# Kernel tuning notes

Hardware: AMD Instinct MI355X
Metric: run time of the kernel (lower is better)

## Reference

```python
import jax, jax.numpy as jnp
import numpy as np

NODE_TYPES = ["patient", "visit", "symptom", "procedure", "disease", "drug"]
N = {"patient": 20000, "visit": 100000, "symptom": 4000, "procedure": 8000,
     "disease": 10000, "drug": 4000}
D = 128          # embedding_dim == hidden_channels
N_LAYERS = 4     # conv1..conv4
# (src, dst) per relation; reverse edges included so every node type gets messages
REL = [("patient", "visit"), ("visit", "patient"),
       ("visit", "symptom"), ("symptom", "visit"),
       ("visit", "procedure"), ("procedure", "visit"),
       ("visit", "disease"), ("disease", "visit"),
       ("visit", "drug"), ("drug", "visit")]
E_FWD = {("patient", "visit"): 100000, ("visit", "symptom"): 300000,
         ("visit", "procedure"): 200000, ("visit", "disease"): 250000,
         ("visit", "drug"): 300000}
EI_NAMES = ["ei_pv", "ei_vp", "ei_vs", "ei_sv", "ei_vpr", "ei_prv",
            "ei_vd", "ei_dv", "ei_vdr", "ei_drv"]
E_LABEL = 200000


def setup_inputs() -> dict:
    key = jax.random.key(0)
    ks = iter(jax.random.split(key, 64))
    inp = {}
    for nt in NODE_TYPES:
        inp[f"node_id_{nt}"] = jnp.arange(N[nt], dtype=jnp.int32)
        inp[f"emb_{nt}"] = jax.random.normal(next(ks), (N[nt], D), jnp.float32)
    for name, (src, dst) in zip(EI_NAMES, REL):
        e = E_FWD.get((src, dst), E_FWD.get((dst, src)))
        row = jax.random.randint(next(ks), (e,), 0, N[src], dtype=jnp.int32)
        col = jax.random.randint(next(ks), (e,), 0, N[dst], dtype=jnp.int32)
        inp[name] = jnp.stack([row, col])
    R = len(REL)
    inp["W_l"] = jax.random.normal(next(ks), (N_LAYERS, R, D, D), jnp.float32) * 0.05
    inp["b_l"] = jnp.zeros((N_LAYERS, R, D), jnp.float32)
    inp["W_r"] = jax.random.normal(next(ks), (N_LAYERS, R, D, D), jnp.float32) * 0.05
    inp["cls_w1"] = jax.random.normal(next(ks), (2 * D, D), jnp.float32) * 0.05
    inp["cls_b1"] = jnp.zeros((D,), jnp.float32)
    inp["cls_w2"] = jax.random.normal(next(ks), (D, 1), jnp.float32) * 0.05
    inp["cls_b2"] = jnp.zeros((1,), jnp.float32)
    row = jax.random.randint(next(ks), (E_LABEL,), 0, N["visit"], dtype=jnp.int32)
    col = jax.random.randint(next(ks), (E_LABEL,), 0, N["drug"], dtype=jnp.int32)
    inp["edge_label_index"] = jnp.stack([row, col])
    inp["edge_label"] = jax.random.bernoulli(next(ks), 0.5, (E_LABEL,)).astype(jnp.float32)
    return inp


def _hetero_sage_layer(x, eis, Wl, bl, Wr):
    # to_hetero semantics: out[dst] = sum over edge types (src,rel,dst) of
    #   SAGEConv_rel: lin_l(mean_j x[src][j]) + lin_r(x[dst])   (PyG defaults)
    out = {nt: jnp.zeros_like(v) for nt, v in x.items()}
    for r, (src, dst) in enumerate(REL):
        ei = eis[r]
        n_dst = x[dst].shape[0]
        msg = jax.ops.segment_sum(x[src][ei[0]], ei[1], num_segments=n_dst)
        deg = jax.ops.segment_sum(jnp.ones((ei.shape[1],), x[src].dtype), ei[1],
                                  num_segments=n_dst)
        mean = msg / jnp.maximum(deg, 1.0)[:, None]  # empty segments stay 0 as in PyG
        out[dst] = out[dst] + mean @ Wl[r] + bl[r] + x[dst] @ Wr[r]
    return out


def reference(node_id_patient, node_id_visit, node_id_symptom, node_id_procedure,
              node_id_disease, node_id_drug,
              emb_patient, emb_visit, emb_symptom, emb_procedure, emb_disease, emb_drug,
              ei_pv, ei_vp, ei_vs, ei_sv, ei_vpr, ei_prv, ei_vd, ei_dv, ei_vdr, ei_drv,
              W_l, b_l, W_r, cls_w1, cls_b1, cls_w2, cls_b2,
              edge_label_index, edge_label):
    x = {"patient": emb_patient[node_id_patient],
         "visit": emb_visit[node_id_visit],
         "symptom": emb_symptom[node_id_symptom],
         "procedure": emb_procedure[node_id_procedure],
         "disease": emb_disease[node_id_disease],
         "drug": emb_drug[node_id_drug]}
    eis = [ei_pv, ei_vp, ei_vs, ei_sv, ei_vpr, ei_prv, ei_vd, ei_dv, ei_vdr, ei_drv]
    for l in range(N_LAYERS):
        x = _hetero_sage_layer(x, eis, W_l[l], b_l[l], W_r[l])
        if l < N_LAYERS - 1:  # relu after conv1..conv3 only; dropout is eval-mode identity
            x = {k: jax.nn.relu(v) for k, v in x.items()}
    # Classifier: gather visit/drug node features per labeled edge, concat, MLP
    zv = x["visit"][edge_label_index[0]]
    zd = x["drug"][edge_label_index[1]]
    h = jax.nn.relu(jnp.concatenate([zv, zd], axis=-1) @ cls_w1 + cls_b1)
    pred = (h @ cls_w2 + cls_b2).reshape(-1)
    # BCE with logits: softplus(z) - z*y, mean-reduced
    loss = jnp.mean(jax.nn.softplus(pred) - pred * edge_label)
    return loss, pred
```

## Files before the change

kernel.cpp:

```cpp
#include <hip/hip_runtime.h>
#include <cmath>


typedef _Float16 f16x8 __attribute__((ext_vector_type(8)));
typedef _Float16 f16x4 __attribute__((ext_vector_type(4)));
typedef float f32x4 __attribute__((ext_vector_type(4)));

#define NREL 10
#define NCOUNTS 546000
#define NEDGES  2300000
#define NVISIT  100000
#define NVEDGES 1150000
#define PLW 546816
#define WT_ELEMS (4 * PLW + 67584)
#define XELEMS 18688000UL
#define SELEMS 5888000UL
#define NBKT 873
#define BCAP 5120

struct GatherMeta { const float* emb[6]; const int* nid[6]; int rows[6]; int off[6]; };
struct AggMeta { const int* rp[5]; _Float16* meanH[5]; _Float16* meanL[5]; int M[5]; };
struct BkMeta {
  const int* ei[NREL]; int E[NREL]; int cbc[NREL]; int ndst[NREL];
  int sh[NREL]; int bb[NREL]; int nb[NREL];
};
struct MTask {
  const _Float16* AH0; const _Float16* AL0;
  const _Float16* AH1; const _Float16* AL1;
  const _Float16* W;
  const float* bias;
  _Float16* outH; _Float16* outL;
  int M, blkOff, K, relu;
};
struct MMeta { MTask t[6]; int nTasks; };

__global__ __launch_bounds__(256) void conv0(GatherMeta g, _Float16* __restrict__ H,
                                             _Float16* __restrict__ L) {
  int t = blockIdx.y;
  int i = blockIdx.x * 256 + threadIdx.x;
  if (i >= g.rows[t] * 16) return;
  int row = i >> 4, q = i & 15;
  int s = g.nid[t][row];
  const float* p = g.emb[t] + (size_t)s * 128 + q * 8;
  float4 v0 = *(const float4*)p;
  float4 v1 = *(const float4*)(p + 4);
  float v[8] = {v0.x, v0.y, v0.z, v0.w, v1.x, v1.y, v1.z, v1.w};
  f16x8 h, l;
  #pragma unroll
  for (int j = 0; j < 8; ++j) {
    h[j] = (_Float16)v[j];
    l[j] = (_Float16)(v[j] - (float)h[j]);
  }
  size_t o = (size_t)(g.off[t] + row) * 128 + q * 8;
  *(f16x8*)(H + o) = h;
  *(f16x8*)(L + o) = l;
}

__global__ __launch_bounds__(256) void bkt_p1(BkMeta bm, int* __restrict__ bcur,
                                              int* __restrict__ bdata) {
  __shared__ int cnt[128];
  __shared__ int base[128];
  __shared__ unsigned short rnk[4096];
  int r = blockIdx.y;
  int E = bm.E[r], sh = bm.sh[r], bb = bm.bb[r], nb = bm.nb[r];
  int tid = threadIdx.x;
  if (tid < 128) cnt[tid] = 0;
  __syncthreads();
  int e0 = blockIdx.x * 4096;
  if (e0 >= E) return;
  const int* dstp = bm.ei[r] + E;
  const int* srcp = bm.ei[r];
  #pragma unroll
  for (int i = 0; i < 16; ++i) {
    int e = e0 + i * 256 + tid;
    if (e < E) {
      int b = dstp[e] >> sh;
      rnk[i * 256 + tid] = (unsigned short)atomicAdd(&cnt[b], 1);
    }
  }
  __syncthreads();
  if (tid < nb && cnt[tid] > 0) base[tid] = atomicAdd(&bcur[bb + tid], cnt[tid]);
  __syncthreads();
  #pragma unroll
  for (int i = 0; i < 16; ++i) {
    int e = e0 + i * 256 + tid;
    if (e < E) {
      int d = dstp[e];
      int b = d >> sh;
      int pos = base[b] + (int)rnk[i * 256 + tid];
      if (pos < BCAP)
        bdata[(size_t)(bb + b) * BCAP + pos] = ((d & ((1 << sh) - 1)) << 17) | srcp[e];
    }
  }
}

__global__ __launch_bounds__(256) void bkt_p2a(BkMeta bm, const int* __restrict__ bcur,
                                               const int* __restrict__ bdata,
                                               int* __restrict__ counts) {
  __shared__ int hist[2048];
  int g = blockIdx.x;
  int r = 0;
  #pragma unroll
  for (int i = 1; i < NREL; ++i) if (g >= bm.bb[i]) r = i;
  int lb = g - bm.bb[r];
  int sh = bm.sh[r], dpb = 1 << sh;
  int tid = threadIdx.x;
  for (int d = tid; d < dpb; d += 256) hist[d] = 0;
  __syncthreads();
  int cnt = bcur[g]; if (cnt > BCAP) cnt = BCAP;
  const int* bd = bdata + (size_t)g * BCAP;
  for (int i = tid; i < cnt; i += 256) atomicAdd(&hist[((unsigned)bd[i]) >> 17], 1);
  __syncthreads();
  int dBase = lb << sh;
  int dMax = bm.ndst[r] - dBase; if (dMax > dpb) dMax = dpb;
  for (int d = tid; d < dMax; d += 256) counts[bm.cbc[r] + dBase + d] = hist[d];
}

__global__ __launch_bounds__(1024) void scan1(const int* __restrict__ counts,
                                              int* __restrict__ partials) {
  __shared__ int s[1024];
  int i = blockIdx.x * 1024 + threadIdx.x;
  s[threadIdx.x] = (i < NCOUNTS) ? counts[i] : 0;
  __syncthreads();
  for (int off = 512; off > 0; off >>= 1) {
    if (threadIdx.x < off) s[threadIdx.x] += s[threadIdx.x + off];
    __syncthreads();
  }
  if (threadIdx.x == 0) partials[blockIdx.x] = s[0];
}

__global__ __launch_bounds__(1024) void scan2(int* __restrict__ partials, int nb) {
  __shared__ int s[1024];
  int t = threadIdx.x;
  int v = (t < nb) ? partials[t] : 0;
  s[t] = v;
  __syncthreads();
  for (int off = 1; off < 1024; off <<= 1) {
    int add = (t >= off) ? s[t - off] : 0;
    __syncthreads();
    s[t] += add;
    __syncthreads();
  }
  if (t < nb) partials[t] = s[t] - v;
}

__global__ __launch_bounds__(1024) void scan3(const int* __restrict__ counts,
                                              int* __restrict__ prefix,
                                              const int* __restrict__ partials) {
  __shared__ int s[1024];
  int t = threadIdx.x;
  int i = blockIdx.x * 1024 + t;
  int v = (i < NCOUNTS) ? counts[i] : 0;
  s[t] = v;
  __syncthreads();
  for (int off = 1; off < 1024; off <<= 1) {
    int add = (t >= off) ? s[t - off] : 0;
    __syncthreads();
    s[t] += add;
    __syncthreads();
  }
  int P = partials[blockIdx.x] + s[t] - v;
  if (i < NCOUNTS) prefix[i] = P;
  if (blockIdx.x == 0 && t == 0) prefix[NCOUNTS] = NEDGES;
}

__global__ __launch_bounds__(256) void bkt_p2b(BkMeta bm, const int* __restrict__ bcur,
                                               const int* __restrict__ bdata,
                                               const int* __restrict__ prefix,
                                               int* __restrict__ esrc) {
  __shared__ int pk[BCAP];
  __shared__ int srt[BCAP];
  __shared__ int cur[2048];
  __shared__ int part[256];
  __shared__ int baseSh;
  int g = blockIdx.x;
  int r = 0;
  #pragma unroll
  for (int i = 1; i < NREL; ++i) if (g >= bm.bb[i]) r = i;
  int lb = g - bm.bb[r];
  int sh = bm.sh[r], dpb = 1 << sh;
  int tid = threadIdx.x;
  int cnt = bcur[g]; if (cnt > BCAP) cnt = BCAP;
  const int* bd = bdata + (size_t)g * BCAP;
  for (int d = tid; d < dpb; d += 256) cur[d] = 0;
  for (int i = tid; i < cnt; i += 256) pk[i] = bd[i];
  __syncthreads();
  for (int i = tid; i < cnt; i += 256) atomicAdd(&cur[((unsigned)pk[i]) >> 17], 1);
  __syncthreads();
  int seg = (dpb + 255) >> 8;
  int s = 0;
  int b0 = tid * seg;
  for (int j = 0; j < seg; ++j) {
    int idx = b0 + j;
    if (idx < dpb) { int v = cur[idx]; cur[idx] = s; s += v; }
  }
  part[tid] = s;
  __syncthreads();
  for (int off = 1; off < 256; off <<= 1) {
    int add = (tid >= off) ? part[tid - off] : 0;
    __syncthreads();
    part[tid] += add;
    __syncthreads();
  }
  int myoff = part[tid] - s;
  for (int j = 0; j < seg; ++j) {
    int idx = b0 + j;
    if (idx < dpb) cur[idx] += myoff;
  }
  if (tid == 0) baseSh = prefix[bm.cbc[r] + (lb << sh)];
  __syncthreads();
  for (int i = tid; i < cnt; i += 256) {
    int p = pk[i];
    int pos = atomicAdd(&cur[((unsigned)p) >> 17], 1);
    srt[pos] = p & 0x1FFFF;
  }
  __syncthreads();
  int base = baseSh;
  for (int i = tid; i < cnt; i += 256) esrc[base + i] = srt[i];
}

__global__ __launch_bounds__(256) void merge_visit(const int* __restrict__ prefix,
                                                   const int* __restrict__ esrc,
                                                   int* __restrict__ mprefix,
                                                   int2* __restrict__ mesrc) {
  const int cbc[5]  = {0, 124000, 232000, 342000, 446000};
  const int yoff[5] = {0, 20000, 24000, 32000, 42000};
  int v = blockIdx.x * 256 + threadIdx.x;
  if (v >= NVISIT) return;
  int e0[5], e1[5];
  int base = 0;
  #pragma unroll
  for (int q = 0; q < 5; ++q) {
    e0[q] = prefix[cbc[q] + v];
    e1[q] = prefix[cbc[q] + v + 1];
    base += e0[q] - prefix[cbc[q]];
  }
  mprefix[v] = base;
  if (v == NVISIT - 1) {
    int t = base;
    #pragma unroll
    for (int q = 0; q < 5; ++q) t += e1[q] - e0[q];
    mprefix[NVISIT] = t;
  }
  int pos = base;
  #pragma unroll
  for (int q = 0; q < 5; ++q) {
    int d = e1[q] - e0[q];
    if (d > 0) {
      int wb = __float_as_int(1.f / (float)d);
      for (int e = e0[q]; e < e1[q]; ++e)
        mesrc[pos++] = make_int2(yoff[q] + esrc[e], wb);
    }
  }
}

__global__ __launch_bounds__(256) void prep_split(
    const float* __restrict__ W_l, const float* __restrict__ b_l,
    const float* __restrict__ W_r, const float* __restrict__ cw1,
    _Float16* __restrict__ Wt, float* __restrict__ visitSumB) {
  const int visitRel[5] = {0, 3, 5, 7, 9};
  const int inRel[5] = {1, 2, 4, 6, 8};
  int gid = blockIdx.x * 256 + threadIdx.x;
  if (gid < 1048576) {
    int l = gid >> 18, o = gid & 262143;
    float val; size_t base; int n, k, Kpad;
    if (o < 163840) {
      int t = o >> 15, e = o & 32767;
      k = e >> 7; n = e & 127; Kpad = 264;
      int r = inRel[t];
      val = (k < 128) ? W_l[(size_t)(l * 10 + r) * 16384 + k * 128 + n]
                      : W_r[(size_t)(l * 10 + r) * 16384 + (k - 128) * 128 + n];
      base = (size_t)l * PLW + t * 67584;
    } else if (o < 245760) {
      int q = (o - 163840) >> 14, e = (o - 163840) & 16383;
      k = e >> 7; n = e & 127; Kpad = 136;
      val = W_l[(size_t)(l * 10 + visitRel[q]) * 16384 + k * 128 + n];
      base = (size_t)l * PLW + 337920 + q * 34816;
    } else {
      int e = o - 245760;
      k = e >> 7; n = e & 127; Kpad = 136;
      val = 0.f;
      #pragma unroll
      for (int q = 0; q < 5; ++q)
        val += W_r[(size_t)(l * 10 + visitRel[q]) * 16384 + k * 128 + n];
      base = (size_t)l * PLW + 512000;
    }
    _Float16 h = (_Float16)val;
    _Float16 lo = (_Float16)(val - (float)h);
    Wt[base + (size_t)n * Kpad + k] = h;
    Wt[base + (size_t)(128 + n) * Kpad + k] = lo;
  } else if (gid < 1081344) {
    int e = gid - 1048576;
    int k = e >> 7, n = e & 127;
    float val = cw1[(size_t)k * 128 + n];
    _Float16 h = (_Float16)val;
    _Float16 lo = (_Float16)(val - (float)h);
    size_t base = (size_t)4 * PLW;
    Wt[base + (size_t)n * 264 + k] = h;
    Wt[base + (size_t)(128 + n) * 264 + k] = lo;
  } else if (gid < 1081856) {
    int e = gid - 1081344;
    int l = e >> 7, c = e & 127;
    float val = 0.f;
    #pragma unroll
    for (int q = 0; q < 5; ++q) val += b_l[(l * 10 + visitRel[q]) * 128 + c];
    visitSumB[e] = val;
  }
}

__global__ __launch_bounds__(256) void agg_small(AggMeta m,
                                                 const _Float16* __restrict__ xvH,
                                                 const int* __restrict__ esrc) {
  int t = blockIdx.y;
  int row = blockIdx.x * 16 + (threadIdx.x >> 4);
  if (row >= m.M[t]) return;
  int q = threadIdx.x & 15;
  const int* rp = m.rp[t];
  int e0 = rp[row], e1 = rp[row + 1];
  float a[8];
  #pragma unroll
  for (int j = 0; j < 8; ++j) a[j] = 0.f;
  int e = e0;
  for (; e + 4 <= e1; e += 4) {
    int s0 = esrc[e], s1 = esrc[e + 1], s2 = esrc[e + 2], s3 = esrc[e + 3];
    f16x8 v0 = *(const f16x8*)(xvH + (size_t)s0 * 128 + q * 8);
    f16x8 v1 = *(const f16x8*)(xvH + (size_t)s1 * 128 + q * 8);
    f16x8 v2 = *(const f16x8*)(xvH + (size_t)s2 * 128 + q * 8);
    f16x8 v3 = *(const f16x8*)(xvH + (size_t)s3 * 128 + q * 8);
    #pragma unroll
    for (int j = 0; j < 8; ++j)
      a[j] += ((float)v0[j] + (float)v1[j]) + ((float)v2[j] + (float)v3[j]);
  }
  for (; e < e1; ++e) {
    int s = esrc[e];
    f16x8 v = *(const f16x8*)(xvH + (size_t)s * 128 + q * 8);
    #pragma unroll
    for (int j = 0; j < 8; ++j) a[j] += (float)v[j];
  }
  float inv = (e1 > e0) ? 1.f / (float)(e1 - e0) : 0.f;
  f16x8 h, l;
  #pragma unroll
  for (int j = 0; j < 8; ++j) {
    float v = a[j] * inv;
    h[j] = (_Float16)v;
    l[j] = (_Float16)(v - (float)h[j]);
  }
  size_t o = (size_t)row * 128 + q * 8;
  *(f16x8*)(m.meanH[t] + o) = h;
  *(f16x8*)(m.meanL[t] + o) = l;
}

__global__ __launch_bounds__(256) void agg_visit(const int* __restrict__ mprefix,
                                                 const int2* __restrict__ mesrc,
                                                 const _Float16* __restrict__ YH,
                                                 _Float16* __restrict__ xvH,
                                                 _Float16* __restrict__ xvL, int doRelu) {
  int row = blockIdx.x * 16 + (threadIdx.x >> 4);
  if (row >= NVISIT) return;
  int q = threadIdx.x & 15;
  size_t o = (size_t)row * 128 + q * 8;
  f16x8 h0 = *(f16x8*)(xvH + o);
  f16x8 l0 = *(f16x8*)(xvL + o);
  float a[8];
  #pragma unroll
  for (int j = 0; j < 8; ++j) a[j] = (float)h0[j] + (float)l0[j];
  int e0 = mprefix[row], e1 = mprefix[row + 1];
  int e = e0;
  for (; e + 4 <= e1; e += 4) {
    int2 p0 = mesrc[e], p1 = mesrc[e + 1], p2 = mesrc[e + 2], p3 = mesrc[e + 3];
    f16x8 v0 = *(const f16x8*)(YH + (size_t)p0.x * 128 + q * 8);
    f16x8 v1 = *(const f16x8*)(YH + (size_t)p1.x * 128 + q * 8);
    f16x8 v2 = *(const f16x8*)(YH + (size_t)p2.x * 128 + q * 8);
    f16x8 v3 = *(const f16x8*)(YH + (size_t)p3.x * 128 + q * 8);
    float w0 = __int_as_float(p0.y), w1 = __int_as_float(p1.y);
    float w2 = __int_as_float(p2.y), w3 = __int_as_float(p3.y);
    #pragma unroll
    for (int j = 0; j < 8; ++j)
      a[j] += (w0 * (float)v0[j] + w1 * (float)v1[j]) +
              (w2 * (float)v2[j] + w3 * (float)v3[j]);
  }
  for (; e < e1; ++e) {
    int2 p = mesrc[e];
    f16x8 v = *(const f16x8*)(YH + (size_t)p.x * 128 + q * 8);
    float w = __int_as_float(p.y);
    #pragma unroll
    for (int j = 0; j < 8; ++j) a[j] += w * (float)v[j];
  }
  f16x8 h, l;
  #pragma unroll
  for (int j = 0; j < 8; ++j) {
    float v = doRelu ? fmaxf(a[j], 0.f) : a[j];
    h[j] = (_Float16)v;
    l[j] = (_Float16)(v - (float)h[j]);
  }
  *(f16x8*)(xvH + o) = h;
  *(f16x8*)(xvL + o) = l;
}

__global__ __launch_bounds__(256, 2) void mgemm(MMeta mm) {
  int b = blockIdx.x;
  int ti = 0;
  for (int i = 1; i < mm.nTasks; ++i) if (b >= mm.t[i].blkOff) ti = i;
  MTask tk = mm.t[ti];
  int blockRow = (b - tk.blkOff) * 128;
  int Kpad = tk.K + 8;

  __shared__ _Float16 Ash[2][128][72];
  int tid = threadIdx.x;
  int wave = tid >> 6, lane = tid & 63;
  int quad = lane >> 4, lm = lane & 15;
  int wr = wave >> 1, wc = wave & 1;

  f32x4 acc[4][4];
  #pragma unroll
  for (int i = 0; i < 4; ++i)
    #pragma unroll
    for (int j = 0; j < 4; ++j) acc[i][j] = (f32x4){0.f, 0.f, 0.f, 0.f};

  const _Float16* wrowH[4];
  const _Float16* wrowL[4];
  #pragma unroll
  for (int nt = 0; nt < 4; ++nt) {
    int n = wc * 64 + nt * 16 + lm;
    wrowH[nt] = tk.W + (size_t)n * Kpad;
    wrowL[nt] = tk.W + (size_t)(128 + n) * Kpad;
  }

  int sr = tid >> 1, sk = (tid & 1) * 32;
  int gr = blockRow + sr; if (gr >= tk.M) gr = tk.M - 1;
  for (int k0 = 0; k0 < tk.K; k0 += 64) {
    const _Float16* AH = (k0 < 128) ? tk.AH0 : tk.AH1;
    const _Float16* AL = (k0 < 128) ? tk.AL0 : tk.AL1;
    size_t abase = (size_t)gr * 128 + (k0 & 127) + sk;
    #pragma unroll
    for (int c = 0; c < 4; ++c) {
      *(f16x8*)&Ash[0][sr][sk + c * 8] = *(const f16x8*)(AH + abase + c * 8);
      *(f16x8*)&Ash[1][sr][sk + c * 8] = *(const f16x8*)(AL + abase + c * 8);
    }
    __syncthreads();
    #pragma unroll
    for (int ks = 0; ks < 64; ks += 32) {
      int kf = k0 + ks + quad * 8;
      f16x8 bh[4], bl[4];
      #pragma unroll
      for (int nt = 0; nt < 4; ++nt) {
        bh[nt] = *(const f16x8*)(wrowH[nt] + kf);
        bl[nt] = *(const f16x8*)(wrowL[nt] + kf);
      }
      #pragma unroll
      for (int mt = 0; mt < 4; ++mt) {
        int r = wr * 64 + mt * 16 + lm;
        f16x8 ah = *(const f16x8*)&Ash[0][r][ks + quad * 8];
        f16x8 al = *(const f16x8*)&Ash[1][r][ks + quad * 8];
        #pragma unroll
        for (int nt = 0; nt < 4; ++nt) {
          acc[mt][nt] = __builtin_amdgcn_mfma_f32_16x16x32_f16(ah, bh[nt], acc[mt][nt], 0, 0, 0);
          acc[mt][nt] = __builtin_amdgcn_mfma_f32_16x16x32_f16(ah, bl[nt], acc[mt][nt], 0, 0, 0);
          acc[mt][nt] = __builtin_amdgcn_mfma_f32_16x16x32_f16(al, bh[nt], acc[mt][nt], 0, 0, 0);
        }
      }
    }
    __syncthreads();
  }

  float bv[4];
  #pragma unroll
  for (int nt = 0; nt < 4; ++nt)
    bv[nt] = tk.bias ? tk.bias[wc * 64 + nt * 16 + lm] : 0.f;
  #pragma unroll
  for (int mt = 0; mt < 4; ++mt) {
    #pragma unroll
    for (int i = 0; i < 4; ++i) {
      int grow = blockRow + wr * 64 + mt * 16 + quad * 4 + i;
      if (grow >= tk.M) continue;
      size_t ob = (size_t)grow * 128 + wc * 64 + lm;
      #pragma unroll
      for (int nt = 0; nt < 4; ++nt) {
        float v = acc[mt][nt][i] + bv[nt];
        if (tk.relu) v = fmaxf(v, 0.f);
        _Float16 h = (_Float16)v;
        tk.outH[ob + nt * 16] = h;
        if (tk.outL) tk.outL[ob + nt * 16] = (_Float16)(v - (float)h);
      }
    }
  }
}

__global__ __launch_bounds__(256, 2) void mgemm_cls(
    const _Float16* __restrict__ xv16, const _Float16* __restrict__ xd16,
    const int* __restrict__ eli, const _Float16* __restrict__ W,
    const float* __restrict__ b1, const float* __restrict__ w2,
    const float* __restrict__ b2, const float* __restrict__ y,
    float* __restrict__ lossOut, float* __restrict__ pred, int M) {
  __shared__ _Float16 Ash[128][72];
  __shared__ int idxA[128];
  __shared__ int idxB[128];
  __shared__ float predPart[128];
  __shared__ float redL[128];
  int tid = threadIdx.x;
  int wave = tid >> 6, lane = tid & 63;
  int quad = lane >> 4, lm = lane & 15;
  int wr = wave >> 1, wc = wave & 1;
  int blockRow = blockIdx.x * 128;
  if (tid < 128) {
    int gr = blockRow + tid;
    idxA[tid] = (gr < M) ? eli[gr] : 0;
  } else {
    int t2 = tid - 128;
    int gr = blockRow + t2;
    idxB[t2] = (gr < M) ? eli[M + gr] : 0;
  }
  f32x4 acc[4][4];
  #pragma unroll
  for (int i = 0; i < 4; ++i)
    #pragma unroll
    for (int j = 0; j < 4; ++j) acc[i][j] = (f32x4){0.f, 0.f, 0.f, 0.f};

  const _Float16* wrowH[4];
  const _Float16* wrowL[4];
  #pragma unroll
  for (int nt = 0; nt < 4; ++nt) {
    int n = wc * 64 + nt * 16 + lm;
    wrowH[nt] = W + (size_t)n * 264;
    wrowL[nt] = W + (size_t)(128 + n) * 264;
  }
  __syncthreads();

  int sr = tid >> 1, sk = (tid & 1) * 32;
  for (int k0 = 0; k0 < 256; k0 += 64) {
    const _Float16* base = (k0 < 128) ? xv16 : xd16;
    int srcRow = (k0 < 128) ? idxA[sr] : idxB[sr];
    const _Float16* p = base + (size_t)srcRow * 128 + (k0 & 127) + sk;
    #pragma unroll
    for (int c = 0; c < 4; ++c)
      *(f16x8*)&Ash[sr][sk + c * 8] = *(const f16x8*)(p + c * 8);
    __syncthreads();
    #pragma unroll
    for (int ks = 0; ks < 64; ks += 32) {
      int kf = k0 + ks + quad * 8;
      f16x8 bh[4], bl[4];
      #pragma unroll
      for (int nt = 0; nt < 4; ++nt) {
        bh[nt] = *(const f16x8*)(wrowH[nt] + kf);
        bl[nt] = *(const f16x8*)(wrowL[nt] + kf);
      }
      #pragma unroll
      for (int mt = 0; mt < 4; ++mt) {
        int r = wr * 64 + mt * 16 + lm;
        f16x8 ah = *(const f16x8*)&Ash[r][ks + quad * 8];
        #pragma unroll
        for (int nt = 0; nt < 4; ++nt) {
          acc[mt][nt] = __builtin_amdgcn_mfma_f32_16x16x32_f16(ah, bh[nt], acc[mt][nt], 0, 0, 0);
          acc[mt][nt] = __builtin_amdgcn_mfma_f32_16x16x32_f16(ah, bl[nt], acc[mt][nt], 0, 0, 0);
        }
      }
    }
    __syncthreads();
  }

  float b1v[4], w2v[4];
  #pragma unroll
  for (int nt = 0; nt < 4; ++nt) {
    int col = wc * 64 + nt * 16 + lm;
    b1v[nt] = b1[col];
    w2v[nt] = w2[col];
  }
  float rowp[4][4];
  #pragma unroll
  for (int mt = 0; mt < 4; ++mt)
    #pragma unroll
    for (int i = 0; i < 4; ++i) {
      float p = 0.f;
      #pragma unroll
      for (int nt = 0; nt < 4; ++nt)
        p += fmaxf(acc[mt][nt][i] + b1v[nt], 0.f) * w2v[nt];
      p += __shfl_xor(p, 1);
      p += __shfl_xor(p, 2);
      p += __shfl_xor(p, 4);
      p += __shfl_xor(p, 8);
      rowp[mt][i] = p;
    }
  if (wc == 0 && lm == 0) {
    #pragma unroll
    for (int mt = 0; mt < 4; ++mt)
      #pragma unroll
      for (int i = 0; i < 4; ++i)
        predPart[wr * 64 + mt * 16 + quad * 4 + i] = rowp[mt][i];
  }
  __syncthreads();
  if (wc == 1 && lm == 0) {
    #pragma unroll
    for (int mt = 0; mt < 4; ++mt)
      #pragma unroll
      for (int i = 0; i < 4; ++i)
        predPart[wr * 64 + mt * 16 + quad * 4 + i] += rowp[mt][i];
  }
  __syncthreads();
  if (tid < 128) {
    int gr = blockRow + tid;
    float lv = 0.f;
    if (gr < M) {
      float z = predPart[tid] + b2[0];
      pred[gr] = z;
      lv = fmaxf(z, 0.f) + log1pf(expf(-fabsf(z))) - z * y[gr];
    }
    redL[tid] = lv;
  }
  __syncthreads();
  if (tid == 0) {
    float s = 0.f;
    for (int i = 0; i < 128; ++i) s += redL[i];
    atomicAdd(lossOut, s * (1.0f / 200000.0f));
  }
}

extern "C" void kernel_launch(void* const* d_in, const int* in_sizes, int n_in,
                              void* d_out, int out_size, void* d_ws, size_t ws_size,
                              hipStream_t stream) {
  static const int kRows[6] = {20000, 100000, 4000, 8000, 10000, 4000};
  static const int kOff[6]  = {0, 20000, 120000, 124000, 132000, 142000};
  static const int kSmallT[5]   = {0, 2, 3, 4, 5};
  static const int kInRel[5]    = {1, 2, 4, 6, 8};
  static const int kCbcIn[5]    = {100000, 120000, 224000, 332000, 442000};
  static const int kYOff[5]     = {0, 20000, 24000, 32000, 42000};
  static const int kBOff[5]     = {0, 157, 189, 252, 331};
  static const int kCbcA[NREL]  = {0, 100000, 120000, 124000, 224000,
                                   232000, 332000, 342000, 442000, 446000};
  static const int kEhA[NREL]   = {100000, 100000, 300000, 300000, 200000,
                                   200000, 250000, 250000, 300000, 300000};
  static const int kNdst[NREL]  = {100000, 20000, 4000, 100000, 8000,
                                   100000, 10000, 100000, 4000, 100000};
  static const int kSh[NREL]    = {11, 9, 5, 10, 7, 10, 7, 10, 5, 10};
  static const int kNB[NREL]    = {49, 40, 125, 98, 63, 98, 79, 98, 125, 98};
  static const int kBB[NREL]    = {0, 49, 89, 214, 312, 375, 473, 552, 650, 775};

  const float* W_l = (const float*)d_in[22];
  const float* b_l = (const float*)d_in[23];
  const float* W_r = (const float*)d_in[24];
  const float* cw1 = (const float*)d_in[25];
  const float* cb1 = (const float*)d_in[26];
  const float* cw2 = (const float*)d_in[27];
  const float* cb2 = (const float*)d_in[28];
  const int* eli = (const int*)d_in[29];
  const float* ylab = (const float*)d_in[30];

  _Float16* H = (_Float16*)d_ws;
  _Float16* L = H + XELEMS;
  _Float16* meanH = L + XELEMS;
  _Float16* meanL = meanH + SELEMS;
  _Float16* YH = meanL + SELEMS;
  _Float16* Wt = YH + SELEMS;
  int* prefix = (int*)(Wt + WT_ELEMS);
  int* counts = prefix + 546004;
  int* esrc = counts + NCOUNTS;
  int* partials = esrc + NEDGES;
  float* visitSumB = (float*)(partials + 1024);
  int* bcur = (int*)(visitSumB + 512);
  int* bdata = bcur + 1024;

  int* mprefix = counts;
  int2* mesrc = (int2*)bdata;

  BkMeta bm;
  for (int r = 0; r < NREL; ++r) {
    bm.ei[r] = (const int*)d_in[12 + r];
    bm.E[r] = kEhA[r];
    bm.cbc[r] = kCbcA[r];
    bm.ndst[r] = kNdst[r];
    bm.sh[r] = kSh[r];
    bm.bb[r] = kBB[r];
    bm.nb[r] = kNB[r];
  }

  hipMemsetAsync(bcur, 0, NBKT * sizeof(int), stream);
  hipMemsetAsync(d_out, 0, sizeof(float), stream);

  prep_split<<<(1081856 + 255) / 256, 256, 0, stream>>>(W_l, b_l, W_r, cw1, Wt, visitSumB);

  GatherMeta gm;
  for (int t = 0; t < 6; ++t) {
    gm.nid[t] = (const int*)d_in[2 * t];
    gm.emb[t] = (const float*)d_in[2 * t + 1];
    gm.rows[t] = kRows[t];
    gm.off[t] = kOff[t];
  }
  conv0<<<dim3(6250, 6), 256, 0, stream>>>(gm, H, L);

  bkt_p1<<<dim3(74, NREL), 256, 0, stream>>>(bm, bcur, bdata);
  bkt_p2a<<<dim3(NBKT), 256, 0, stream>>>(bm, bcur, bdata, counts);
  scan1<<<534, 1024, 0, stream>>>(counts, partials);
  scan2<<<1, 1024, 0, stream>>>(partials, 534);
  scan3<<<534, 1024, 0, stream>>>(counts, prefix, partials);
  bkt_p2b<<<dim3(NBKT), 256, 0, stream>>>(bm, bcur, bdata, prefix, esrc);
  merge_visit<<<dim3((NVISIT + 255) / 256), 256, 0, stream>>>(prefix, esrc, mprefix, mesrc);

  _Float16* xvH = H + (size_t)kOff[1] * 128;
  _Float16* xvL = L + (size_t)kOff[1] * 128;

  for (int l = 0; l < 4; ++l) {
    int doRelu = (l < 3);
    int last = (l == 3);
    _Float16* LW = Wt + (size_t)l * PLW;

    AggMeta am;
    if (!last) {
      for (int t = 0; t < 5; ++t) {
        am.rp[t] = prefix + kCbcIn[t];
        am.meanH[t] = meanH + (size_t)kYOff[t] * 128;
        am.meanL[t] = meanL + (size_t)kYOff[t] * 128;
        am.M[t] = kRows[kSmallT[t]];
      }
      agg_small<<<dim3(1250, 5), 256, 0, stream>>>(am, xvH, esrc);
    } else {
      am.rp[0] = prefix + kCbcIn[4];
      am.meanH[0] = meanH + (size_t)kYOff[4] * 128;
      am.meanL[0] = meanL + (size_t)kYOff[4] * 128;
      am.M[0] = 4000;
      agg_small<<<dim3(250, 1), 256, 0, stream>>>(am, xvH, esrc);
    }

    MMeta m2;
    m2.nTasks = 6;
    for (int q = 0; q < 5; ++q) {
      size_t so = (size_t)kOff[kSmallT[q]] * 128;
      m2.t[q].AH0 = H + so; m2.t[q].AL0 = L + so;
      m2.t[q].AH1 = nullptr; m2.t[q].AL1 = nullptr;
      m2.t[q].W = LW + 337920 + (size_t)q * 34816;
      m2.t[q].bias = nullptr;
      m2.t[q].outH = YH + (size_t)kYOff[q] * 128;
      m2.t[q].outL = nullptr;
      m2.t[q].M = kRows[kSmallT[q]];
      m2.t[q].blkOff = kBOff[q];
      m2.t[q].K = 128;
      m2.t[q].relu = 0;
    }
    m2.t[5].AH0 = xvH; m2.t[5].AL0 = xvL;
    m2.t[5].AH1 = nullptr; m2.t[5].AL1 = nullptr;
    m2.t[5].W = LW + 512000;
    m2.t[5].bias = visitSumB + l * 128;
    m2.t[5].outH = xvH; m2.t[5].outL = xvL;
    m2.t[5].M = NVISIT;
    m2.t[5].blkOff = 363;
    m2.t[5].K = 128;
    m2.t[5].relu = 0;
    mgemm<<<dim3(363 + 782), 256, 0, stream>>>(m2);

    MMeta m1;
    if (!last) {
      m1.nTasks = 5;
      for (int t = 0; t < 5; ++t) {
        size_t mo = (size_t)kYOff[t] * 128;
        size_t so = (size_t)kOff[kSmallT[t]] * 128;
        m1.t[t].AH0 = meanH + mo; m1.t[t].AL0 = meanL + mo;
        m1.t[t].AH1 = H + so;     m1.t[t].AL1 = L + so;
        m1.t[t].W = LW + (size_t)t * 67584;
        m1.t[t].bias = b_l + (size_t)(l * 10 + kInRel[t]) * 128;
        m1.t[t].outH = H + so;    m1.t[t].outL = L + so;
        m1.t[t].M = kRows[kSmallT[t]];
        m1.t[t].blkOff = kBOff[t];
        m1.t[t].K = 256;
        m1.t[t].relu = doRelu;
      }
      mgemm<<<dim3(363), 256, 0, stream>>>(m1);
    } else {
      size_t mo = (size_t)kYOff[4] * 128;
      size_t so = (size_t)kOff[5] * 128;
      m1.nTasks = 1;
      m1.t[0].AH0 = meanH + mo; m1.t[0].AL0 = meanL + mo;
      m1.t[0].AH1 = H + so;     m1.t[0].AL1 = L + so;
      m1.t[0].W = LW + (size_t)4 * 67584;
      m1.t[0].bias = b_l + (size_t)(l * 10 + kInRel[4]) * 128;
      m1.t[0].outH = H + so;    m1.t[0].outL = L + so;
      m1.t[0].M = 4000;
      m1.t[0].blkOff = 0;
      m1.t[0].K = 256;
      m1.t[0].relu = 0;
      mgemm<<<dim3(32), 256, 0, stream>>>(m1);
    }

    agg_visit<<<dim3(6250), 256, 0, stream>>>(mprefix, mesrc, YH, xvH, xvL, doRelu);
  }

  const int ML = 200000;
  mgemm_cls<<<dim3((ML + 127) / 128), 256, 0, stream>>>(
      xvH, H + (size_t)kOff[5] * 128, eli, Wt + (size_t)4 * PLW, cb1, cw2, cb2, ylab,
      (float*)d_out, (float*)d_out + 1, ML);
}
```

Measured before the change: 925.2 us.

## Factor classifier first layer into per-node projections before edge gather

The concat-then-matmul classifier is split algebraically into concat(zv,zd)@W1 = zv@W1[:128] + zd@W1[128:]. The projections are computed once per visit node (100k) and drug node (4k) with the existing mgemm, so the per-edge kernel only gathers two projected rows, adds them, applies relu and the w2 dot product. This replaces the 200k-row gathered GEMM with a 104k-row GEMM plus a light gather/reduce kernel. The cost is extra workspace for the projected hi/lo buffers, which are aliased onto existing scratch regions (prefix, meanH), and BCAP is reduced to fit the layout.

```diff
diff --git a/kernel.cpp b/kernel.cpp
--- a/kernel.cpp
+++ b/kernel.cpp
@@ -3,7 +3,6 @@
 
 
 typedef _Float16 f16x8 __attribute__((ext_vector_type(8)));
-typedef _Float16 f16x4 __attribute__((ext_vector_type(4)));
 typedef float f32x4 __attribute__((ext_vector_type(4)));
 
 #define NREL 10
@@ -12,11 +11,11 @@
 #define NVISIT  100000
 #define NVEDGES 1150000
 #define PLW 546816
-#define WT_ELEMS (4 * PLW + 67584)
+#define WT_ELEMS (4 * PLW + 69632)
 #define XELEMS 18688000UL
 #define SELEMS 5888000UL
 #define NBKT 873
-#define BCAP 5120
+#define BCAP 5056
 
 struct GatherMeta { const float* emb[6]; const int* nid[6]; int rows[6]; int off[6]; };
 struct AggMeta { const int* rp[5]; _Float16* meanH[5]; _Float16* meanL[5]; int M[5]; };
@@ -295,9 +294,10 @@
     float val = cw1[(size_t)k * 128 + n];
     _Float16 h = (_Float16)val;
     _Float16 lo = (_Float16)(val - (float)h);
-    size_t base = (size_t)4 * PLW;
-    Wt[base + (size_t)n * 264 + k] = h;
-    Wt[base + (size_t)(128 + n) * 264 + k] = lo;
+    size_t base = (size_t)4 * PLW + (k < 128 ? 0 : 34816);
+    int kk = k & 127;
+    Wt[base + (size_t)n * 136 + kk] = h;
+    Wt[base + (size_t)(128 + n) * 136 + kk] = lo;
   } else if (gid < 1081856) {
     int e = gid - 1081344;
     int l = e >> 7, c = e & 127;
@@ -486,132 +486,56 @@
   }
 }
 
-__global__ __launch_bounds__(256, 2) void mgemm_cls(
-    const _Float16* __restrict__ xv16, const _Float16* __restrict__ xd16,
-    const int* __restrict__ eli, const _Float16* __restrict__ W,
-    const float* __restrict__ b1, const float* __restrict__ w2,
+__global__ __launch_bounds__(256) void cls_edge(
+    const _Float16* __restrict__ UH, const _Float16* __restrict__ UL,
+    const _Float16* __restrict__ VH, const _Float16* __restrict__ VL,
+    const int* __restrict__ eli, const float* __restrict__ w2,
     const float* __restrict__ b2, const float* __restrict__ y,
     float* __restrict__ lossOut, float* __restrict__ pred, int M) {
-  __shared__ _Float16 Ash[128][72];
-  __shared__ int idxA[128];
-  __shared__ int idxB[128];
-  __shared__ float predPart[128];
-  __shared__ float redL[128];
+  __shared__ float lsum[4];
   int tid = threadIdx.x;
-  int wave = tid >> 6, lane = tid & 63;
-  int quad = lane >> 4, lm = lane & 15;
-  int wr = wave >> 1, wc = wave & 1;
-  int blockRow = blockIdx.x * 128;
-  if (tid < 128) {
-    int gr = blockRow + tid;
-    idxA[tid] = (gr < M) ? eli[gr] : 0;
-  } else {
-    int t2 = tid - 128;
-    int gr = blockRow + t2;
-    idxB[t2] = (gr < M) ? eli[M + gr] : 0;
-  }
-  f32x4 acc[4][4];
-  #pragma unroll
-  for (int i = 0; i < 4; ++i)
-    #pragma unroll
-    for (int j = 0; j < 4; ++j) acc[i][j] = (f32x4){0.f, 0.f, 0.f, 0.f};
-
-  const _Float16* wrowH[4];
-  const _Float16* wrowL[4];
-  #pragma unroll
-  for (int nt = 0; nt < 4; ++nt) {
-    int n = wc * 64 + nt * 16 + lm;
-    wrowH[nt] = W + (size_t)n * 264;
-    wrowL[nt] = W + (size_t)(128 + n) * 264;
-  }
-  __syncthreads();
-
-  int sr = tid >> 1, sk = (tid & 1) * 32;
-  for (int k0 = 0; k0 < 256; k0 += 64) {
-    const _Float16* base = (k0 < 128) ? xv16 : xd16;
-    int srcRow = (k0 < 128) ? idxA[sr] : idxB[sr];
-    const _Float16* p = base + (size_t)srcRow * 128 + (k0 & 127) + sk;
-    #pragma unroll
-    for (int c = 0; c < 4; ++c)
-      *(f16x8*)&Ash[sr][sk + c * 8] = *(const f16x8*)(p + c * 8);
-    __syncthreads();
-    #pragma unroll
-    for (int ks = 0; ks < 64; ks += 32) {
-      int kf = k0 + ks + quad * 8;
-      f16x8 bh[4], bl[4];
+  int q = tid & 15;
+  int lane = tid & 63;
+  float w2v[8];
+  #pragma unroll
+  for (int j = 0; j < 8; ++j) w2v[j] = w2[q * 8 + j];
+  float bias = b2[0];
+  float lacc = 0.f;
+  int e0 = blockIdx.x * 128 + (tid >> 4);
+  #pragma unroll
+  for (int p = 0; p < 8; ++p) {
+    int e = e0 + p * 16;
+    if (e < M) {
+      int vi = eli[e], di = eli[M + e];
+      size_t uo = (size_t)vi * 128 + q * 8;
+      size_t vo = (size_t)di * 128 + q * 8;
+      f16x8 uh = *(const f16x8*)(UH + uo);
+      f16x8 ul = *(const f16x8*)(UL + uo);
+      f16x8 vh = *(const f16x8*)(VH + vo);
+      f16x8 vl = *(const f16x8*)(VL + vo);
+      float part = 0.f;
       #pragma unroll
-      for (int nt = 0; nt < 4; ++nt) {
-        bh[nt] = *(const f16x8*)(wrowH[nt] + kf);
-        bl[nt] = *(const f16x8*)(wrowL[nt] + kf);
+      for (int j = 0; j < 8; ++j) {
+        float t = ((float)uh[j] + (float)ul[j]) + ((float)vh[j] + (float)vl[j]);
+        part += fmaxf(t, 0.f) * w2v[j];
       }
-      #pragma unroll
-      for (int mt = 0; mt < 4; ++mt) {
-        int r = wr * 64 + mt * 16 + lm;
-        f16x8 ah = *(const f16x8*)&Ash[r][ks + quad * 8];
-        #pragma unroll
-        for (int nt = 0; nt < 4; ++nt) {
-          acc[mt][nt] = __builtin_amdgcn_mfma_f32_16x16x32_f16(ah, bh[nt], acc[mt][nt], 0, 0, 0);
-          acc[mt][nt] = __builtin_amdgcn_mfma_f32_16x16x32_f16(ah, bl[nt], acc[mt][nt], 0, 0, 0);
-        }
+      part += __shfl_xor(part, 1);
+      part += __shfl_xor(part, 2);
+      part += __shfl_xor(part, 4);
+      part += __shfl_xor(part, 8);
+      if (q == 0) {
+        float z = part + bias;
+        pred[e] = z;
+        lacc += fmaxf(z, 0.f) + log1pf(expf(-fabsf(z))) - z * y[e];
       }
     }
-    __syncthreads();
-  }
-
-  float b1v[4], w2v[4];
-  #pragma unroll
-  for (int nt = 0; nt < 4; ++nt) {
-    int col = wc * 64 + nt * 16 + lm;
-    b1v[nt] = b1[col];
-    w2v[nt] = w2[col];
-  }
-  float rowp[4][4];
-  #pragma unroll
-  for (int mt = 0; mt < 4; ++mt)
-    #pragma unroll
-    for (int i = 0; i < 4; ++i) {
-      float p = 0.f;
-      #pragma unroll
-      for (int nt = 0; nt < 4; ++nt)
-        p += fmaxf(acc[mt][nt][i] + b1v[nt], 0.f) * w2v[nt];
-      p += __shfl_xor(p, 1);
-      p += __shfl_xor(p, 2);
-      p += __shfl_xor(p, 4);
-      p += __shfl_xor(p, 8);
-      rowp[mt][i] = p;
-    }
-  if (wc == 0 && lm == 0) {
-    #pragma unroll
-    for (int mt = 0; mt < 4; ++mt)
-      #pragma unroll
-      for (int i = 0; i < 4; ++i)
-        predPart[wr * 64 + mt * 16 + quad * 4 + i] = rowp[mt][i];
-  }
-  __syncthreads();
-  if (wc == 1 && lm == 0) {
-    #pragma unroll
-    for (int mt = 0; mt < 4; ++mt)
-      #pragma unroll
-      for (int i = 0; i < 4; ++i)
-        predPart[wr * 64 + mt * 16 + quad * 4 + i] += rowp[mt][i];
-  }
-  __syncthreads();
-  if (tid < 128) {
-    int gr = blockRow + tid;
-    float lv = 0.f;
-    if (gr < M) {
-      float z = predPart[tid] + b2[0];
-      pred[gr] = z;
-      lv = fmaxf(z, 0.f) + log1pf(expf(-fabsf(z))) - z * y[gr];
-    }
-    redL[tid] = lv;
-  }
-  __syncthreads();
-  if (tid == 0) {
-    float s = 0.f;
-    for (int i = 0; i < 128; ++i) s += redL[i];
-    atomicAdd(lossOut, s * (1.0f / 200000.0f));
-  }
+  }
+  lacc += __shfl_xor(lacc, 16);
+  lacc += __shfl_xor(lacc, 32);
+  if (lane == 0) lsum[tid >> 6] = lacc;
+  __syncthreads();
+  if (tid == 0)
+    atomicAdd(lossOut, (lsum[0] + lsum[1] + lsum[2] + lsum[3]) * (1.0f / 200000.0f));
 }
 
 extern "C" void kernel_launch(void* const* d_in, const int* in_sizes, int n_in,
@@ -660,6 +584,11 @@
 
   int* mprefix = counts;
   int2* mesrc = (int2*)bdata;
+
+  _Float16* UH = meanH;
+  _Float16* VH = meanH + (size_t)NVISIT * 128;
+  _Float16* VL = VH + (size_t)4000 * 128;
+  _Float16* UL = (_Float16*)prefix;
 
   BkMeta bm;
   for (int r = 0; r < NREL; ++r) {
@@ -781,8 +710,30 @@
     agg_visit<<<dim3(6250), 256, 0, stream>>>(mprefix, mesrc, YH, xvH, xvL, doRelu);
   }
 
+  MMeta muv;
+  muv.nTasks = 2;
+  muv.t[0].AH0 = xvH; muv.t[0].AL0 = xvL;
+  muv.t[0].AH1 = nullptr; muv.t[0].AL1 = nullptr;
+  muv.t[0].W = Wt + (size_t)4 * PLW;
+  muv.t[0].bias = cb1;
+  muv.t[0].outH = UH; muv.t[0].outL = UL;
+  muv.t[0].M = NVISIT;
+  muv.t[0].blkOff = 0;
+  muv.t[0].K = 128;
+  muv.t[0].relu = 0;
+  muv.t[1].AH0 = H + (size_t)kOff[5] * 128; muv.t[1].AL0 = L + (size_t)kOff[5] * 128;
+  muv.t[1].AH1 = nullptr; muv.t[1].AL1 = nullptr;
+  muv.t[1].W = Wt + (size_t)4 * PLW + 34816;
+  muv.t[1].bias = nullptr;
+  muv.t[1].outH = VH; muv.t[1].outL = VL;
+  muv.t[1].M = 4000;
+  muv.t[1].blkOff = 782;
+  muv.t[1].K = 128;
+  muv.t[1].relu = 0;
+  mgemm<<<dim3(782 + 32), 256, 0, stream>>>(muv);
+
   const int ML = 200000;
-  mgemm_cls<<<dim3((ML + 127) / 128), 256, 0, stream>>>(
-      xvH, H + (size_t)kOff[5] * 128, eli, Wt + (size_t)4 * PLW, cb1, cw2, cb2, ylab,
+  cls_edge<<<dim3((ML + 127) / 128), 256, 0, stream>>>(
+      UH, UL, VH, VL, eli, cw2, cb2, ylab,
       (float*)d_out, (float*)d_out + 1, ML);
 }
```

Result: no change. 943.0 us (+1.9%).
